# Kernel optimization log

Hardware: AMD Instinct MI355X
Metric: run time of the kernel (lower is better)

Reference implementation:

```python
import jax, jax.numpy as jnp
import numpy as np


def setup_inputs() -> dict:
    key = jax.random.key(0)
    k1, k2 = jax.random.split(key)
    B, T, D = 16, 2048, 1024
    inputs = jax.random.normal(k1, (B, T, D), dtype=jnp.float32)
    mask = jax.random.randint(k2, (B, T), 0, 2).astype(bool)
    return {"inputs": inputs, "mask": mask}


def reference(inputs, mask):
    """Batched stream compaction (JIT-compatible ragged representation).

    Original TF layer loops over the batch and, per sample, gathers the
    rows of inputs[i] where mask[i] is True, returning ragged lists of
    (collected_values, valid_indices). Since JAX requires static shapes,
    we return the padded-compacted equivalent:
      collected: [B, T, D]  valid rows moved to the front (order preserved),
                            invalid tail zeroed.
      valid_idx: [B, T]     original timestep index of each collected row,
                            -1 in the padded tail.
      counts:    [B]        number of valid rows per sample, i.e.
                            collected[i, :counts[i]] == ragged segment i.
    """
    # Stable argsort of the inverted mask puts valid positions first,
    # preserving their original order -> single-pass prefix-sum compaction.
    order = jnp.argsort(jnp.logical_not(mask), axis=1, stable=True)      # [B, T]
    sorted_valid = jnp.take_along_axis(mask, order, axis=1)              # [B, T]
    collected = jnp.take_along_axis(inputs, order[:, :, None], axis=1)   # [B, T, D]
    collected = jnp.where(sorted_valid[:, :, None], collected, 0.0)
    valid_idx = jnp.where(sorted_valid, order, -1)
    counts = jnp.sum(mask, axis=1)
    return collected, valid_idx, counts
```

## Files before the change

kernel.cpp:

```cpp
#include <hip/hip_runtime.h>


#define BB 16
#define TT 2048
#define DD 1024
#define ROW4 (DD / 4)

typedef float f4 __attribute__((ext_vector_type(4)));

__global__ __launch_bounds__(256) void scan_kernel(
    const int* __restrict__ mask,
    float* __restrict__ out_vidx,
    float* __restrict__ out_counts,
    int* __restrict__ ws_src,
    int* __restrict__ ws_cnt)
{
    const int b = blockIdx.x;
    const int tid = threadIdx.x;
    const int4* m4 = (const int4*)(mask + b * TT);

    int4 a0 = m4[tid * 2];
    int4 a1 = m4[tid * 2 + 1];
    int vals[8];
    vals[0] = (a0.x != 0); vals[1] = (a0.y != 0);
    vals[2] = (a0.z != 0); vals[3] = (a0.w != 0);
    vals[4] = (a1.x != 0); vals[5] = (a1.y != 0);
    vals[6] = (a1.z != 0); vals[7] = (a1.w != 0);
    int s = 0;
#pragma unroll
    for (int i = 0; i < 8; ++i) s += vals[i];

    __shared__ int sdata[256];
    sdata[tid] = s;
    __syncthreads();
#pragma unroll
    for (int off = 1; off < 256; off <<= 1) {
        int v = (tid >= off) ? sdata[tid - off] : 0;
        __syncthreads();
        sdata[tid] += v;
        __syncthreads();
    }
    const int excl = sdata[tid] - s;
    const int total = sdata[255];

    int pos = excl;
#pragma unroll
    for (int i = 0; i < 8; ++i) {
        if (vals[i]) {
            const int t = tid * 8 + i;
            ws_src[b * TT + pos] = t;
            out_vidx[b * TT + pos] = (float)t;
            ++pos;
        }
    }

    for (int c = total + tid; c < TT; c += 256) {
        out_vidx[b * TT + c] = -1.0f;
    }

    if (tid == 0) {
        ws_cnt[b] = total;
        out_counts[b] = (float)total;
    }
}

__global__ __launch_bounds__(256) void gather_kernel(
    const f4* __restrict__ in,
    const int* __restrict__ ws_src,
    const int* __restrict__ ws_cnt,
    f4* __restrict__ out)
{
    const int tid  = threadIdx.x;
    const int lrow = tid >> 5;
    const int lane = tid & 31;
    const int row  = blockIdx.x * 8 + lrow;
    const int b    = row >> 11;
    const int c    = row & (TT - 1);

    f4* dst = out + (size_t)row * ROW4;
    if (c < ws_cnt[b]) {
        const int src = ws_src[row];
        const f4* sp = in + ((size_t)(b << 11) + (size_t)src) * ROW4;
        f4 v[8];
#pragma unroll
        for (int j = 0; j < 8; ++j)
            v[j] = __builtin_nontemporal_load(sp + lane + j * 32);
#pragma unroll
        for (int j = 0; j < 8; ++j)
            __builtin_nontemporal_store(v[j], dst + lane + j * 32);
    } else {
        const f4 z = {0.f, 0.f, 0.f, 0.f};
#pragma unroll
        for (int j = 0; j < 8; ++j)
            __builtin_nontemporal_store(z, dst + lane + j * 32);
    }
}

extern "C" void kernel_launch(void* const* d_in, const int* in_sizes, int n_in,
                              void* d_out, int out_size, void* d_ws, size_t ws_size,
                              hipStream_t stream) {
    const float* inputs = (const float*)d_in[0];
    const int* mask = (const int*)d_in[1];

    float* out = (float*)d_out;
    float* out_collected = out;
    float* out_vidx = out + (size_t)BB * TT * DD;
    float* out_counts = out_vidx + (size_t)BB * TT;

    int* ws_src = (int*)d_ws;
    int* ws_cnt = ws_src + BB * TT;

    scan_kernel<<<BB, 256, 0, stream>>>(mask, out_vidx, out_counts, ws_src, ws_cnt);
    gather_kernel<<<BB * TT / 8, 256, 0, stream>>>(
        (const f4*)inputs, ws_src, ws_cnt, (f4*)out_collected);
}
```

Measured before the change: 218.0 us.

## Fuse scan and gather into one kernel with per-block redundant mask scan

Merges the per-batch scan kernel and the gather kernel into a single launch. Each block of 16 rows rescans the whole 2048-entry mask for its batch using wave shuffles instead of a shared-memory scan, then scatters its own source rows to their compacted destinations (scatter instead of gather). This removes the second launch, the workspace round trip and the serial dependency on a 16-block scan. In exchange every block repeats the full mask scan, and rows now follow a scatter pattern, with the zero tail written by position.

```diff
diff --git a/kernel.cpp b/kernel.cpp
--- a/kernel.cpp
+++ b/kernel.cpp
@@ -5,94 +5,89 @@
 #define TT 2048
 #define DD 1024
 #define ROW4 (DD / 4)
+#define RPB 16
+#define CHUNKS (TT / RPB)
 
 typedef float f4 __attribute__((ext_vector_type(4)));
 
-__global__ __launch_bounds__(256) void scan_kernel(
+__global__ __launch_bounds__(256) void fused_compact_kernel(
+    const f4* __restrict__ in,
     const int* __restrict__ mask,
+    f4* __restrict__ out,
     float* __restrict__ out_vidx,
-    float* __restrict__ out_counts,
-    int* __restrict__ ws_src,
-    int* __restrict__ ws_cnt)
+    float* __restrict__ out_counts)
 {
-    const int b = blockIdx.x;
-    const int tid = threadIdx.x;
+    const int tid   = threadIdx.x;
+    const int b     = blockIdx.x >> 7;
+    const int chunk = blockIdx.x & (CHUNKS - 1);
+    const int t0    = chunk * RPB;
+
     const int4* m4 = (const int4*)(mask + b * TT);
-
     int4 a0 = m4[tid * 2];
     int4 a1 = m4[tid * 2 + 1];
-    int vals[8];
-    vals[0] = (a0.x != 0); vals[1] = (a0.y != 0);
-    vals[2] = (a0.z != 0); vals[3] = (a0.w != 0);
-    vals[4] = (a1.x != 0); vals[5] = (a1.y != 0);
-    vals[6] = (a1.z != 0); vals[7] = (a1.w != 0);
+    int v[8];
+    v[0] = (a0.x != 0); v[1] = (a0.y != 0); v[2] = (a0.z != 0); v[3] = (a0.w != 0);
+    v[4] = (a1.x != 0); v[5] = (a1.y != 0); v[6] = (a1.z != 0); v[7] = (a1.w != 0);
+    int pre[8];
     int s = 0;
 #pragma unroll
-    for (int i = 0; i < 8; ++i) s += vals[i];
+    for (int i = 0; i < 8; ++i) { pre[i] = s; s += v[i]; }
 
-    __shared__ int sdata[256];
-    sdata[tid] = s;
+    int incl = s;
+#pragma unroll
+    for (int off = 1; off < 64; off <<= 1) {
+        int n = __shfl_up(incl, off, 64);
+        if ((tid & 63) >= off) incl += n;
+    }
+
+    __shared__ int wsum[4];
+    __shared__ int l_dst[RPB];
+    if ((tid & 63) == 63) wsum[tid >> 6] = incl;
     __syncthreads();
+    int woff = 0;
+    const int wid = tid >> 6;
 #pragma unroll
-    for (int off = 1; off < 256; off <<= 1) {
-        int v = (tid >= off) ? sdata[tid - off] : 0;
-        __syncthreads();
-        sdata[tid] += v;
-        __syncthreads();
-    }
-    const int excl = sdata[tid] - s;
-    const int total = sdata[255];
+    for (int w = 0; w < 4; ++w) woff += (w < wid) ? wsum[w] : 0;
+    const int total = wsum[0] + wsum[1] + wsum[2] + wsum[3];
+    const int excl_base = woff + incl - s;
 
-    int pos = excl;
+    const int first_tid = t0 >> 3;
+    if (tid == first_tid || tid == first_tid + 1) {
+        const int base_li = (tid - first_tid) * 8;
 #pragma unroll
-    for (int i = 0; i < 8; ++i) {
-        if (vals[i]) {
-            const int t = tid * 8 + i;
-            ws_src[b * TT + pos] = t;
-            out_vidx[b * TT + pos] = (float)t;
-            ++pos;
+        for (int i = 0; i < 8; ++i) {
+            const int dst = v[i] ? (excl_base + pre[i]) : -1;
+            l_dst[base_li + i] = dst;
+            if (dst >= 0) out_vidx[b * TT + dst] = (float)(tid * 8 + i);
         }
     }
+    if (chunk == 0 && tid == 0) out_counts[b] = (float)total;
+    __syncthreads();
 
-    for (int c = total + tid; c < TT; c += 256) {
-        out_vidx[b * TT + c] = -1.0f;
+    const int lrow = tid >> 4;
+    const int lane = tid & 15;
+    const int t    = t0 + lrow;
+    const int dst  = l_dst[lrow];
+    const size_t inbase = (size_t)b * TT;
+
+    if (dst >= 0) {
+        const f4* sp = in + (inbase + (size_t)t) * ROW4 + lane;
+        f4* dp = out + (inbase + (size_t)dst) * ROW4 + lane;
+        f4 vv[16];
+#pragma unroll
+        for (int j = 0; j < 16; ++j)
+            vv[j] = __builtin_nontemporal_load(sp + j * 16);
+#pragma unroll
+        for (int j = 0; j < 16; ++j)
+            __builtin_nontemporal_store(vv[j], dp + j * 16);
     }
-
-    if (tid == 0) {
-        ws_cnt[b] = total;
-        out_counts[b] = (float)total;
-    }
-}
-
-__global__ __launch_bounds__(256) void gather_kernel(
-    const f4* __restrict__ in,
-    const int* __restrict__ ws_src,
-    const int* __restrict__ ws_cnt,
-    f4* __restrict__ out)
-{
-    const int tid  = threadIdx.x;
-    const int lrow = tid >> 5;
-    const int lane = tid & 31;
-    const int row  = blockIdx.x * 8 + lrow;
-    const int b    = row >> 11;
-    const int c    = row & (TT - 1);
-
-    f4* dst = out + (size_t)row * ROW4;
-    if (c < ws_cnt[b]) {
-        const int src = ws_src[row];
-        const f4* sp = in + ((size_t)(b << 11) + (size_t)src) * ROW4;
-        f4 v[8];
-#pragma unroll
-        for (int j = 0; j < 8; ++j)
-            v[j] = __builtin_nontemporal_load(sp + lane + j * 32);
-#pragma unroll
-        for (int j = 0; j < 8; ++j)
-            __builtin_nontemporal_store(v[j], dst + lane + j * 32);
-    } else {
+    if (t >= total) {
+        f4* dp = out + (inbase + (size_t)t) * ROW4 + lane;
         const f4 z = {0.f, 0.f, 0.f, 0.f};
 #pragma unroll
-        for (int j = 0; j < 8; ++j)
-            __builtin_nontemporal_store(z, dst + lane + j * 32);
+        for (int j = 0; j < 16; ++j)
+            __builtin_nontemporal_store(z, dp + j * 16);
+        if (lane == 0) out_vidx[b * TT + t] = -1.0f;
     }
 }
 
@@ -107,10 +102,6 @@
     float* out_vidx = out + (size_t)BB * TT * DD;
     float* out_counts = out_vidx + (size_t)BB * TT;
 
-    int* ws_src = (int*)d_ws;
-    int* ws_cnt = ws_src + BB * TT;
-
-    scan_kernel<<<BB, 256, 0, stream>>>(mask, out_vidx, out_counts, ws_src, ws_cnt);
-    gather_kernel<<<BB * TT / 8, 256, 0, stream>>>(
-        (const f4*)inputs, ws_src, ws_cnt, (f4*)out_collected);
+    fused_compact_kernel<<<BB * CHUNKS, 256, 0, stream>>>(
+        (const f4*)inputs, mask, (f4*)out_collected, out_vidx, out_counts);
 }
```

Result: no change. 219.2 us (+0.5%).
